# Kernel tuning notes

Measured on AMD Instinct MI355X. Metric: run time of the kernel, lower is better.

## Reference

```python
import jax, jax.numpy as jnp
import numpy as np

N, F, K = 2048, 256, 4
E = 65536

def setup_inputs() -> dict:
    key = jax.random.key(0)
    ks = jax.random.split(key, 8)
    batch_x = jax.random.normal(ks[0], (N, F), dtype=jnp.float32)
    # eigen-matrix of a normalized Laplacian is diagonal in practice, but the
    # original code treats it as a dense [N,N] operand; we mimic a diagonal
    # eigenvalue matrix (eigenvalues in [0,2]) -- math is identical either way.
    lam_diag = 2.0 * jax.random.uniform(ks[1], (N,), dtype=jnp.float32)
    batch_lam = jnp.diag(lam_diag)
    batch_U = jax.random.normal(ks[2], (N, N), dtype=jnp.float32) / jnp.sqrt(jnp.float32(N))
    # init.uniform_(a, 0, 2) / (b, 0, 2) / (c, -1, 1); keep a-b bounded away from 0
    a_list = 1.0 + jax.random.uniform(ks[3], (K,), dtype=jnp.float32)        # [1,2)
    b_list = 0.9 * jax.random.uniform(ks[4], (K,), dtype=jnp.float32)       # [0,0.9)
    c_list = 2.0 * jax.random.uniform(ks[5], (K,), dtype=jnp.float32) - 1.0  # [-1,1)
    residual_alpha = jnp.ones((1,), dtype=jnp.float32)
    edge_index = jax.random.randint(ks[6], (2, E), 0, N, dtype=jnp.int64)
    return {"batch_x": batch_x, "batch_lam": batch_lam, "batch_U": batch_U,
            "a_list": a_list, "b_list": b_list, "c_list": c_list,
            "residual_alpha": residual_alpha, "edge_index": edge_index}

def reference(batch_x, batch_lam, batch_U, a_list, b_list, c_list, residual_alpha, edge_index):
    n = batch_lam.shape[0]
    I = jnp.eye(n, dtype=batch_lam.dtype)
    out = residual_alpha * batch_x  # residual added at hop 0 in original
    for i in range(a_list.shape[0]):
        # filter_rep = (a_i*I - Lam) @ (Lam - b_i*I), then relu
        rep = (a_list[i] * I - batch_lam) @ (batch_lam - b_list[i] * I)
        rep = jax.nn.relu(rep)
        scale = c_list[i] / ((a_list[i] - b_list[i]) * (a_list[i] - b_list[i]) / 4.0)
        filt = scale * (batch_U @ (rep @ (batch_U.T @ batch_x)))
        out = out + filt
    return out
```

## Files before the change

kernel.cpp:

```cpp
#include <hip/hip_runtime.h>
#include <type_traits>

typedef unsigned short u16;
typedef __attribute__((ext_vector_type(8))) short short8;
typedef __attribute__((ext_vector_type(4))) float floatx4;

__device__ __forceinline__ u16 f2u(float f) {
  unsigned int x = __float_as_uint(f);
  x += 0x7fff + ((x >> 16) & 1);
  return (u16)(x >> 16);
}

__device__ __forceinline__ void async16(const void* g, void* l) {
  __builtin_amdgcn_global_load_lds(
      (const __attribute__((address_space(1))) unsigned int*)g,
      (__attribute__((address_space(3))) unsigned int*)l, 16, 0, 0);
}

__global__ __launch_bounds__(256) void prep_kernel(
    const float* __restrict__ U, const float* __restrict__ x,
    u16* __restrict__ Ut, u16* __restrict__ Ubf, u16* __restrict__ xT,
    int N, int F) {
  __shared__ __attribute__((aligned(16))) float tile[64][65];
  int bb = blockIdx.x;
  int t = threadIdx.x;

  const float* in;
  u16 *outT, *outC;
  int R, C, c0, r0;
  if (bb < 1024) {
    in = U; outT = Ut; outC = Ubf; R = N; C = N;
    c0 = (bb & 31) * 64; r0 = (bb >> 5) * 64;
  } else {
    int b2 = bb - 1024;
    in = x; outT = xT; outC = nullptr; R = N; C = F;
    c0 = (b2 & 3) * 64; r0 = (b2 >> 2) * 64;
  }

#pragma unroll
  for (int p = 0; p < 4; ++p) {
    int e = p * 256 + t;
    int row = e >> 4, col = (e & 15) * 4;
    float4 v = *(const float4*)(in + (size_t)(r0 + row) * C + c0 + col);
    tile[row][col] = v.x;
    tile[row][col + 1] = v.y;
    tile[row][col + 2] = v.z;
    tile[row][col + 3] = v.w;
    if (outC) {
      union { uint2 u; u16 s[4]; } pk;
      pk.s[0] = f2u(v.x); pk.s[1] = f2u(v.y);
      pk.s[2] = f2u(v.z); pk.s[3] = f2u(v.w);
      *(uint2*)(outC + (size_t)(r0 + row) * C + c0 + col) = pk.u;
    }
  }
  __syncthreads();
#pragma unroll
  for (int p = 0; p < 2; ++p) {
    int e = p * 256 + t;
    int orow = e >> 3, oc = (e & 7) * 8;
    union { uint4 v; u16 s[8]; } tmp;
#pragma unroll
    for (int i = 0; i < 8; ++i) tmp.s[i] = f2u(tile[oc + i][orow]);
    *(uint4*)(outT + (size_t)(c0 + orow) * R + r0 + oc) = tmp.v;
  }
}

template <bool SCALE_D, bool RESIDUAL, typename CT>
__global__ __launch_bounds__(256) void gemm32(
    const u16* __restrict__ A, const u16* __restrict__ B, CT* __restrict__ C,
    int M, int NN, int K, const float* __restrict__ lam,
    const float* __restrict__ pa, const float* __restrict__ pb,
    const float* __restrict__ pc, const float* __restrict__ resid,
    const float* __restrict__ alpha_p) {
  __shared__ __attribute__((aligned(16))) u16 lA[2 * 4 * 32 * 32];
  __shared__ __attribute__((aligned(16))) u16 lB[2 * 4 * 32 * 32];
  const int m0 = blockIdx.x * 32;
  const int n0 = blockIdx.y * 32;
  const int t = threadIdx.x;
  const int wave = t >> 6, lane = t & 63;
  const int wm = wave >> 1, wn = wave & 1;
  const int q = lane >> 4, l15 = lane & 15;

  const int within = t & 127, st0 = t >> 7;
  const u16* gA = A + (size_t)(m0 + (within >> 2)) * K + (within & 3) * 8;
  const u16* gB = B + (size_t)(n0 + (within >> 2)) * K + (within & 3) * 8;
  char* lAc = (char*)lA;
  char* lBc = (char*)lB;

  const int NM = K >> 7;

  auto issue = [&](int i, int buf) {
    int k0 = i * 128;
    async16(gA + k0 + st0 * 32, lAc + buf * 8192 + t * 16);
    async16(gA + k0 + (st0 + 2) * 32, lAc + buf * 8192 + 4096 + t * 16);
    async16(gB + k0 + st0 * 32, lBc + buf * 8192 + t * 16);
    async16(gB + k0 + (st0 + 2) * 32, lBc + buf * 8192 + 4096 + t * 16);
  };

  floatx4 acc = (floatx4){0.f, 0.f, 0.f, 0.f};

  issue(0, 0);
  for (int i = 0; i < NM; ++i) {
    const int buf = i & 1;
    __syncthreads();
    if (i + 1 < NM) issue(i + 1, buf ^ 1);
    const u16* lAb = lA + buf * 4096;
    const u16* lBb = lB + buf * 4096;
#pragma unroll
    for (int st = 0; st < 4; ++st) {
      short8 af = *(const short8*)&lAb[st * 1024 + (wm * 16 + l15) * 32 + q * 8];
      short8 bf = *(const short8*)&lBb[st * 1024 + (wn * 16 + l15) * 32 + q * 8];
      acc = __builtin_amdgcn_mfma_f32_16x16x32_bf16(af, bf, acc, 0, 0, 0);
    }
  }

  const int col = n0 + wn * 16 + l15;
  float ds = 1.f;
  if (SCALE_D) {
    float lv = lam[(size_t)col * NN + col];
    float dacc = 0.f;
#pragma unroll
    for (int i = 0; i < 4; ++i) {
      float ai = pa[i], bi = pb[i], ci = pc[i];
      float rep = (ai - lv) * (lv - bi);
      rep = rep > 0.f ? rep : 0.f;
      dacc += ci * 4.f / ((ai - bi) * (ai - bi)) * rep;
    }
    ds = dacc;
  }
  float alpha = 0.f;
  if (RESIDUAL) alpha = alpha_p[0];
  const int rbase = m0 + wm * 16 + q * 4;
#pragma unroll
  for (int r = 0; r < 4; ++r) {
    float v = acc[r];
    if (SCALE_D) v *= ds;
    size_t idx = (size_t)(rbase + r) * NN + col;
    if (RESIDUAL) v += alpha * resid[idx];
    if constexpr (std::is_same<CT, u16>::value)
      C[idx] = f2u(v);
    else
      C[idx] = v;
  }
}

extern "C" void kernel_launch(void* const* d_in, const int* in_sizes, int n_in,
                              void* d_out, int out_size, void* d_ws,
                              size_t ws_size, hipStream_t stream) {
  const int N = 2048, F = 256;
  const float* x = (const float*)d_in[0];
  const float* lam = (const float*)d_in[1];
  const float* U = (const float*)d_in[2];
  const float* a = (const float*)d_in[3];
  const float* b = (const float*)d_in[4];
  const float* c = (const float*)d_in[5];
  const float* alpha = (const float*)d_in[6];

  char* ws = (char*)d_ws;
  u16* xT = (u16*)ws;
  u16* Ut = (u16*)(ws + (1 << 20));
  u16* Ubf = (u16*)(ws + (9 << 20));
  u16* zT = (u16*)(ws + (17 << 20));

  prep_kernel<<<1152, 256, 0, stream>>>(U, x, Ut, Ubf, xT, N, F);
  gemm32<true, false, u16><<<dim3(F / 32, N / 32), 256, 0, stream>>>(
      xT, Ut, zT, F, N, N, lam, a, b, c, nullptr, nullptr);
  gemm32<false, true, float><<<dim3(N / 32, F / 32), 256, 0, stream>>>(
      Ubf, zT, (float*)d_out, N, F, N, nullptr, nullptr, nullptr, nullptr,
      x, alpha);
}
```

Before: 114.2 us.

## Split K across waves in 32x32 GEMM with LDS reduction and vectorized epilogue

Each of the four waves now computes the full 32x32 output tile over its own K-substep, holding four MFMA accumulators, instead of each wave owning one 16x16 quadrant across all substeps. Partial sums go to LDS and are reduced by all threads. The epilogue then writes float4 or packed bf16 stores and loads the residual as float4. The intent is to reuse each loaded fragment across two MFMAs, halve LDS fragment reads per MFMA, and coalesce the output stores. In exchange it adds 16KB of LDS, an extra barrier and an LDS reduction pass.

```diff
diff --git a/kernel.cpp b/kernel.cpp
--- a/kernel.cpp
+++ b/kernel.cpp
@@ -66,19 +66,19 @@
 }
 
 template <bool SCALE_D, bool RESIDUAL, typename CT>
-__global__ __launch_bounds__(256) void gemm32(
+__global__ __launch_bounds__(256) void gemm32ks(
     const u16* __restrict__ A, const u16* __restrict__ B, CT* __restrict__ C,
     int M, int NN, int K, const float* __restrict__ lam,
     const float* __restrict__ pa, const float* __restrict__ pb,
     const float* __restrict__ pc, const float* __restrict__ resid,
     const float* __restrict__ alpha_p) {
-  __shared__ __attribute__((aligned(16))) u16 lA[2 * 4 * 32 * 32];
-  __shared__ __attribute__((aligned(16))) u16 lB[2 * 4 * 32 * 32];
+  __shared__ __attribute__((aligned(16))) u16 lA[2 * 4096];
+  __shared__ __attribute__((aligned(16))) u16 lB[2 * 4096];
+  __shared__ __attribute__((aligned(16))) float accf[4 * 1024];
   const int m0 = blockIdx.x * 32;
   const int n0 = blockIdx.y * 32;
   const int t = threadIdx.x;
   const int wave = t >> 6, lane = t & 63;
-  const int wm = wave >> 1, wn = wave & 1;
   const int q = lane >> 4, l15 = lane & 15;
 
   const int within = t & 127, st0 = t >> 7;
@@ -97,50 +97,79 @@
     async16(gB + k0 + (st0 + 2) * 32, lBc + buf * 8192 + 4096 + t * 16);
   };
 
-  floatx4 acc = (floatx4){0.f, 0.f, 0.f, 0.f};
+  floatx4 acc[2][2];
+#pragma unroll
+  for (int i = 0; i < 2; ++i)
+#pragma unroll
+    for (int j = 0; j < 2; ++j) acc[i][j] = (floatx4){0.f, 0.f, 0.f, 0.f};
 
   issue(0, 0);
   for (int i = 0; i < NM; ++i) {
     const int buf = i & 1;
     __syncthreads();
     if (i + 1 < NM) issue(i + 1, buf ^ 1);
-    const u16* lAb = lA + buf * 4096;
-    const u16* lBb = lB + buf * 4096;
-#pragma unroll
-    for (int st = 0; st < 4; ++st) {
-      short8 af = *(const short8*)&lAb[st * 1024 + (wm * 16 + l15) * 32 + q * 8];
-      short8 bf = *(const short8*)&lBb[st * 1024 + (wn * 16 + l15) * 32 + q * 8];
-      acc = __builtin_amdgcn_mfma_f32_16x16x32_bf16(af, bf, acc, 0, 0, 0);
+    const u16* lAb = lA + buf * 4096 + wave * 1024;
+    const u16* lBb = lB + buf * 4096 + wave * 1024;
+    short8 a0 = *(const short8*)&lAb[l15 * 32 + q * 8];
+    short8 a1 = *(const short8*)&lAb[(16 + l15) * 32 + q * 8];
+    short8 b0 = *(const short8*)&lBb[l15 * 32 + q * 8];
+    short8 b1 = *(const short8*)&lBb[(16 + l15) * 32 + q * 8];
+    acc[0][0] = __builtin_amdgcn_mfma_f32_16x16x32_bf16(a0, b0, acc[0][0], 0, 0, 0);
+    acc[0][1] = __builtin_amdgcn_mfma_f32_16x16x32_bf16(a0, b1, acc[0][1], 0, 0, 0);
+    acc[1][0] = __builtin_amdgcn_mfma_f32_16x16x32_bf16(a1, b0, acc[1][0], 0, 0, 0);
+    acc[1][1] = __builtin_amdgcn_mfma_f32_16x16x32_bf16(a1, b1, acc[1][1], 0, 0, 0);
+  }
+
+  __syncthreads();
+#pragma unroll
+  for (int mt = 0; mt < 2; ++mt)
+#pragma unroll
+    for (int nt = 0; nt < 2; ++nt)
+#pragma unroll
+      for (int r = 0; r < 4; ++r)
+        accf[wave * 1024 + (mt * 16 + q * 4 + r) * 32 + nt * 16 + l15] =
+            acc[mt][nt][r];
+  __syncthreads();
+
+  const int e = t * 4;
+  float4 s0 = *(const float4*)&accf[e];
+  float4 s1 = *(const float4*)&accf[1024 + e];
+  float4 s2 = *(const float4*)&accf[2048 + e];
+  float4 s3 = *(const float4*)&accf[3072 + e];
+  float v[4] = {s0.x + s1.x + s2.x + s3.x, s0.y + s1.y + s2.y + s3.y,
+                s0.z + s1.z + s2.z + s3.z, s0.w + s1.w + s2.w + s3.w};
+  const int row = e >> 5, colb = e & 31;
+  const size_t base = (size_t)(m0 + row) * NN + n0 + colb;
+  if (SCALE_D) {
+#pragma unroll
+    for (int j = 0; j < 4; ++j) {
+      int col = n0 + colb + j;
+      float lv = lam[(size_t)col * NN + col];
+      float dacc = 0.f;
+#pragma unroll
+      for (int i = 0; i < 4; ++i) {
+        float ai = pa[i], bi = pb[i], ci = pc[i];
+        float rep = (ai - lv) * (lv - bi);
+        rep = rep > 0.f ? rep : 0.f;
+        dacc += ci * 4.f / ((ai - bi) * (ai - bi)) * rep;
+      }
+      v[j] *= dacc;
     }
   }
-
-  const int col = n0 + wn * 16 + l15;
-  float ds = 1.f;
-  if (SCALE_D) {
-    float lv = lam[(size_t)col * NN + col];
-    float dacc = 0.f;
-#pragma unroll
-    for (int i = 0; i < 4; ++i) {
-      float ai = pa[i], bi = pb[i], ci = pc[i];
-      float rep = (ai - lv) * (lv - bi);
-      rep = rep > 0.f ? rep : 0.f;
-      dacc += ci * 4.f / ((ai - bi) * (ai - bi)) * rep;
-    }
-    ds = dacc;
-  }
-  float alpha = 0.f;
-  if (RESIDUAL) alpha = alpha_p[0];
-  const int rbase = m0 + wm * 16 + q * 4;
-#pragma unroll
-  for (int r = 0; r < 4; ++r) {
-    float v = acc[r];
-    if (SCALE_D) v *= ds;
-    size_t idx = (size_t)(rbase + r) * NN + col;
-    if (RESIDUAL) v += alpha * resid[idx];
-    if constexpr (std::is_same<CT, u16>::value)
-      C[idx] = f2u(v);
-    else
-      C[idx] = v;
+  if (RESIDUAL) {
+    float alpha = alpha_p[0];
+    float4 rx = *(const float4*)(resid + base);
+    v[0] += alpha * rx.x; v[1] += alpha * rx.y;
+    v[2] += alpha * rx.z; v[3] += alpha * rx.w;
+  }
+  if constexpr (std::is_same<CT, u16>::value) {
+    union { uint2 u; u16 s[4]; } pk;
+    pk.s[0] = f2u(v[0]); pk.s[1] = f2u(v[1]);
+    pk.s[2] = f2u(v[2]); pk.s[3] = f2u(v[3]);
+    *(uint2*)(C + base) = pk.u;
+  } else {
+    float4 o = {v[0], v[1], v[2], v[3]};
+    *(float4*)(C + base) = o;
   }
 }
 
@@ -163,9 +192,9 @@
   u16* zT = (u16*)(ws + (17 << 20));
 
   prep_kernel<<<1152, 256, 0, stream>>>(U, x, Ut, Ubf, xT, N, F);
-  gemm32<true, false, u16><<<dim3(F / 32, N / 32), 256, 0, stream>>>(
+  gemm32ks<true, false, u16><<<dim3(F / 32, N / 32), 256, 0, stream>>>(
       xT, Ut, zT, F, N, N, lam, a, b, c, nullptr, nullptr);
-  gemm32<false, true, float><<<dim3(N / 32, F / 32), 256, 0, stream>>>(
+  gemm32ks<false, true, float><<<dim3(N / 32, F / 32), 256, 0, stream>>>(
       Ubf, zT, (float*)d_out, N, F, N, nullptr, nullptr, nullptr, nullptr,
       x, alpha);
 }
```

New measurement: 116.5 us. 2.0% more time.
